# Kernel tuning notes

Measured on AMD Instinct MI355X. Metric: run time of the kernel, lower is better.

The kernel has to match this reference:

```python
import jax, jax.numpy as jnp
import numpy as np

TOP_K = 32
LN_EPS = 1e-5
NORM_EPS = 1e-12


def _l2_normalize(x):
    # matches F.normalize(x, dim=-1): x / max(||x||_2, eps)
    n = jnp.sqrt(jnp.sum(x * x, axis=-1, keepdims=True))
    return x / jnp.maximum(n, NORM_EPS)


def setup_inputs() -> dict:
    key = jax.random.key(0)
    k1, k2, k3 = jax.random.split(key, 3)
    N, M, D = 8192, 32768, 1024
    return {
        "query": jax.random.normal(k1, (N, D), dtype=jnp.float32),
        "memory_keys": jax.random.normal(k2, (M, D), dtype=jnp.float32) * 0.1,
        "memory_values": jax.random.normal(k3, (M, D), dtype=jnp.float32) * 0.1,
        "temperature": jnp.asarray(1.0 / np.sqrt(D), dtype=jnp.float32),
        "ln_gamma": jnp.ones((D,), dtype=jnp.float32),
        "ln_beta": jnp.zeros((D,), dtype=jnp.float32),
    }


def reference(query, memory_keys, memory_values, temperature, ln_gamma, ln_beta):
    qn = _l2_normalize(query)                       # [N, D]
    kn = _l2_normalize(memory_keys)                 # [M, D]
    sim = jnp.einsum("nd,md->nm", qn, kn) * jnp.abs(temperature)  # [N, M]
    top_scores, top_idx = jax.lax.top_k(sim, TOP_K)               # [N, K]
    attn = jax.nn.softmax(top_scores, axis=-1)                    # [N, K]
    selected = memory_values[top_idx]                             # [N, K, D]
    retrieved = jnp.einsum("nk,nkd->nd", attn, selected)          # [N, D]
    x = retrieved + query
    mu = jnp.mean(x, axis=-1, keepdims=True)
    var = jnp.mean((x - mu) ** 2, axis=-1, keepdims=True)
    out = (x - mu) * jax.lax.rsqrt(var + LN_EPS) * ln_gamma + ln_beta
    return out, attn
```

## Files before the change

### kernel.cpp

```cpp
#include <hip/hip_runtime.h>
#include <hip/hip_bf16.h>

#define D 1024
#define NQ 8192
#define NM 32768
#define TOPK 32
#define NBXT 256

typedef __attribute__((ext_vector_type(8))) __bf16 bf16x8;
typedef __attribute__((ext_vector_type(4))) float f32x4;
typedef __attribute__((ext_vector_type(2))) long longx2;

__device__ __forceinline__ void load_lds16(const void* g, void* l) {
  __builtin_amdgcn_global_load_lds(
      (const __attribute__((address_space(1))) void*)g,
      (__attribute__((address_space(3))) void*)l, 16, 0, 0);
}

__device__ __forceinline__ ushort f2bf(float f) {
  unsigned u = __float_as_uint(f);
  unsigned r = (u + 0x7FFFu + ((u >> 16) & 1u)) >> 16;
  return (ushort)r;
}
__device__ __forceinline__ unsigned key16(unsigned u) {
  return u ^ ((u & 0x8000u) ? 0xFFFFu : 0x8000u);
}
__device__ __forceinline__ float bf2f(ushort u) {
  return __uint_as_float(((unsigned)u) << 16);
}

#define FP8_SCALE 32.0f
#define INV_ACC (1.0f / 1024.0f)

__global__ __launch_bounds__(256) void norm_cast8_k(const float* __restrict__ in,
                                                    unsigned* __restrict__ out8) {
  const int row = blockIdx.x;
  const int tid = threadIdx.x;
  const float4 v = ((const float4*)(in + (size_t)row * D))[tid];
  float ss = v.x * v.x + v.y * v.y + v.z * v.z + v.w * v.w;
#pragma unroll
  for (int off = 32; off; off >>= 1) ss += __shfl_xor(ss, off, 64);
  __shared__ float wsum[4];
  const int wid = tid >> 6, lane = tid & 63;
  if (lane == 0) wsum[wid] = ss;
  __syncthreads();
  const float tot = wsum[0] + wsum[1] + wsum[2] + wsum[3];
  const float inv = FP8_SCALE / fmaxf(sqrtf(tot), 1e-12f);
  int r = __builtin_amdgcn_cvt_pk_fp8_f32(v.x * inv, v.y * inv, 0, false);
  r = __builtin_amdgcn_cvt_pk_fp8_f32(v.z * inv, v.w * inv, r, true);
  const int w5 = tid & 31, blk = tid >> 5;
  const int g = w5 >> 1;
  const int h = g >> 2, l4g = g & 3;
  const int G = (h >> 1) * 8 + l4g * 2 + (h & 1);
  out8[(size_t)row * 256 + blk * 32 + G * 2 + (w5 & 1)] = (unsigned)r;
}

__global__ __launch_bounds__(256) void cast_v_k(const float* __restrict__ in,
                                                ushort* __restrict__ out) {
  const int row = blockIdx.x;
  const int tid = threadIdx.x;
  const float4 v = ((const float4*)(in + (size_t)row * D))[tid];
  ushort4 o;
  o.x = f2bf(v.x);
  o.y = f2bf(v.y);
  o.z = f2bf(v.z);
  o.w = f2bf(v.w);
  ((ushort4*)(out + (size_t)row * D))[tid] = o;
}

__global__ __launch_bounds__(256, 4) void gemm128(const uchar* __restrict__ A8,
                                                  const uchar* __restrict__ B8,
                                                  ushort* __restrict__ C,
                                                  ushort* __restrict__ TM,
                                                  int nby, int srows) {
  __shared__ alignas(16) ushort lds[16384];
  __shared__ float wmax[2][128];
  uchar* const As = (uchar*)lds;
  uchar* const Bs = (uchar*)lds + 16384;
  const int tid = threadIdx.x;
  const int lane = tid & 63, wid = tid >> 6;
  const int l15 = lane & 15, l4 = lane >> 4;

  const int nwg = (int)gridDim.x;
  const int q = nwg >> 3, r = nwg & 7;
  const int xcd = (int)blockIdx.x & 7, pos = (int)blockIdx.x >> 3;
  const int wg = (xcd < r ? xcd * (q + 1) : r * (q + 1) + (xcd - r) * q) + pos;
  const int bx = wg / nby, by = wg % nby;

  const int wr = wid >> 1, wc = wid & 1;

  f32x4 acc[4][4];
#pragma unroll
  for (int m = 0; m < 4; m++)
#pragma unroll
    for (int n = 0; n < 4; n++) acc[m][n] = f32x4{0.f, 0.f, 0.f, 0.f};

  const int srow = tid >> 3;
  const int cc = ((tid & 7) ^ ((tid >> 3) & 7)) << 4;
  const uchar* gA = A8 + ((size_t)by * 128 + srow) * 1024 + cc;
  const uchar* gB = B8 + ((size_t)bx * 128 + srow) * 1024 + cc;
  uchar* const ldsA = As + wid * 1024;
  uchar* const ldsB = Bs + wid * 1024;

  const int ob0 = (((0 + l4) ^ (l15 & 7)) << 4);
  const int ob1 = (((4 + l4) ^ (l15 & 7)) << 4);
  const uchar* const abase = As + (wr * 64 + l15) * 128;
  const uchar* const bbase = Bs + (wc * 64 + l15) * 128;

#pragma unroll 1
  for (int kt = 0; kt < 8; ++kt) {
    const int ko = kt * 128;
#pragma unroll
    for (int l = 0; l < 4; ++l) {
      load_lds16(gA + (size_t)l * 32 * 1024 + ko, ldsA + l * 4096);
      load_lds16(gB + (size_t)l * 32 * 1024 + ko, ldsB + l * 4096);
    }
    __syncthreads();
#pragma unroll
    for (int hp = 0; hp < 2; ++hp) {
      const int ob = hp ? ob1 : ob0;
      longx2 af[4], bfv[4];
#pragma unroll
      for (int m = 0; m < 4; ++m) af[m] = *(const longx2*)(abase + m * 2048 + ob);
#pragma unroll
      for (int n = 0; n < 4; ++n) bfv[n] = *(const longx2*)(bbase + n * 2048 + ob);
#pragma unroll
      for (int m = 0; m < 4; ++m)
#pragma unroll
        for (int n = 0; n < 4; ++n) {
          acc[m][n] = __builtin_amdgcn_mfma_f32_16x16x32_fp8_fp8(af[m].x, bfv[n].x, acc[m][n], 0, 0, 0);
          acc[m][n] = __builtin_amdgcn_mfma_f32_16x16x32_fp8_fp8(af[m].y, bfv[n].y, acc[m][n], 0, 0, 0);
        }
    }
    __syncthreads();
  }

#pragma unroll
  for (int m = 0; m < 4; ++m)
#pragma unroll
    for (int j = 0; j < 4; ++j) {
      float fm = fmaxf(fmaxf(acc[m][0][j], acc[m][1][j]), fmaxf(acc[m][2][j], acc[m][3][j]));
#pragma unroll
      for (int off = 1; off < 16; off <<= 1) fm = fmaxf(fm, __shfl_xor(fm, off, 64));
      if (l15 == 0) wmax[wc][wr * 64 + l4 * 4 + m * 16 + j] = fm;
    }
  __syncthreads();
  if (tid < 128) {
    const float fm = fmaxf(wmax[0][tid], wmax[1][tid]) * INV_ACC;
    TM[(size_t)bx * srows + by * 128 + tid] = (ushort)key16((unsigned)f2bf(fm));
  }

#pragma unroll
  for (int m = 0; m < 4; ++m)
#pragma unroll
    for (int n = 0; n < 4; ++n) {
      const int col = wc * 64 + n * 16 + l15;
      const int c8 = col >> 3, c7 = col & 7;
#pragma unroll
      for (int j = 0; j < 4; ++j) {
        const int row = wr * 64 + m * 16 + l4 * 4 + j;
        lds[row * 128 + ((c8 ^ (row & 7)) << 3) + c7] = f2bf(acc[m][n][j] * INV_ACC);
      }
    }
  __syncthreads();
  const int orow = tid >> 4, seg = tid & 15;
#pragma unroll
  for (int p = 0; p < 8; ++p) {
    const int row = p * 16 + orow;
    const bf16x8 v = *(const bf16x8*)&lds[row * 128 + ((seg ^ (row & 7)) << 3)];
    *(bf16x8*)&C[((size_t)by * 128 + row) * NM + bx * 128 + seg * 8] = v;
  }
}

#define CAP2 1024
__global__ __launch_bounds__(512) void topk_k(const ushort* __restrict__ scores,
                                              const ushort* __restrict__ tmax,
                                              int srows, int row_base,
                                              const float* __restrict__ temp,
                                              float* __restrict__ attn,
                                              int* __restrict__ idx_out) {
  const int lrow = blockIdx.x;
  const int grow = row_base + lrow;
  const int tid = threadIdx.x;
  const int lane = tid & 63, wid = tid >> 6;
  __shared__ unsigned tlb_s, M_s;
  __shared__ int nqt_s, cnt_s;
  __shared__ ushort qt[NBXT];
  __shared__ unsigned ckey[CAP2];
  __shared__ unsigned cand64[64];
  __shared__ unsigned okey[TOPK];
  __shared__ int oidx[TOPK];

  if (tid == 0) cnt_s = 0;

  if (tid < 64) {
    const unsigned k0 = tmax[(size_t)lane * srows + lrow];
    const unsigned k1 = tmax[(size_t)(lane + 64) * srows + lrow];
    const unsigned k2 = tmax[(size_t)(lane + 128) * srows + lrow];
    const unsigned k3 = tmax[(size_t)(lane + 192) * srows + lrow];
    unsigned mx = max(max(k0, k1), max(k2, k3));
#pragma unroll
    for (int off = 32; off; off >>= 1) mx = max(mx, __shfl_xor(mx, off, 64));
    unsigned lo = 0, hi = mx;
    while (lo < hi) {
      const unsigned mid = (lo + hi + 1) >> 1;
      int c = (int)(k0 >= mid) + (int)(k1 >= mid) + (int)(k2 >= mid) + (int)(k3 >= mid);
#pragma unroll
      for (int off = 32; off; off >>= 1) c += __shfl_xor(c, off, 64);
      if (c >= TOPK) lo = mid; else hi = mid - 1;
    }
    int base = 0;
    {
      const bool p = k0 >= lo;
      const unsigned long long bm = __ballot(p);
      if (p) qt[base + __popcll(bm & ((1ull << lane) - 1ull))] = (ushort)lane;
      base += __popcll(bm);
    }
    {
      const bool p = k1 >= lo;
      const unsigned long long bm = __ballot(p);
      if (p) qt[base + __popcll(bm & ((1ull << lane) - 1ull))] = (ushort)(lane + 64);
      base += __popcll(bm);
    }
    {
      const bool p = k2 >= lo;
      const unsigned long long bm = __ballot(p);
      if (p) qt[base + __popcll(bm & ((1ull << lane) - 1ull))] = (ushort)(lane + 128);
      base += __popcll(bm);
    }
    {
      const bool p = k3 >= lo;
      const unsigned long long bm = __ballot(p);
      if (p) qt[base + __popcll(bm & ((1ull << lane) - 1ull))] = (ushort)(lane + 192);
      base += __popcll(bm);
    }
    if (lane == 0) { nqt_s = base; tlb_s = lo; M_s = mx; }
  }
  __syncthreads();
  const unsigned M = M_s;
  const int nqt = nqt_s;
  unsigned t0 = tlb_s;
  unsigned tlo = t0, thi = M;

  const unsigned* rowu = (const unsigned*)(scores + (size_t)lrow * NM);
  int cnt = 0;
  for (int att = 0; att < 18; ++att) {
    for (int i = wid; i < nqt; i += 8) {
      const int tb = qt[i];
      const unsigned u = rowu[tb * 64 + lane];
      const unsigned m = (u >> 15) & 0x00010001u;
      const unsigned kk = u ^ (m * 0x7FFFu + 0x80008000u);
      const unsigned klo = kk & 0xFFFFu, khi = kk >> 16;
      const int bidx = tb * 128 + lane * 2;
      if (klo >= t0) { const int qq = atomicAdd(&cnt_s, 1); if (qq < CAP2) ckey[qq] = (klo << 16) | (unsigned)(32767 - bidx); }
      if (khi >= t0) { const int qq = atomicAdd(&cnt_s, 1); if (qq < CAP2) ckey[qq] = (khi << 16) | (unsigned)(32767 - (bidx + 1)); }
    }
    __syncthreads();
    cnt = cnt_s;
    __syncthreads();
    if ((cnt >= TOPK && cnt <= CAP2) || att == 17) break;
    if (cnt > CAP2) { tlo = t0; t0 = t0 + ((thi - t0 + 1) >> 1); }
    else { thi = t0; t0 = tlo + ((t0 - tlo) >> 1); }
    if (tid == 0) cnt_s = 0;
    __syncthreads();
  }
  const int n = min(cnt, CAP2);

  if (tid < 64) {
    unsigned lo = t0, hi = M;
    while (lo < hi) {
      const unsigned mid = (lo + hi + 1) >> 1;
      int c = 0;
      for (int i = lane; i < n; i += 64) c += (int)((ckey[i] >> 16) >= mid);
#pragma unroll
      for (int off = 32; off; off >>= 1) c += __shfl_xor(c, off, 64);
      if (c >= TOPK) lo = mid; else hi = mid - 1;
    }
    const unsigned t32 = lo;
    int c32 = 0;
    for (int i = lane; i < n; i += 64) c32 += (int)((ckey[i] >> 16) >= t32);
#pragma unroll
    for (int off = 32; off; off >>= 1) c32 += __shfl_xor(c32, off, 64);

    if (c32 <= 64) {
      cand64[lane] = 0;
      int base = 0;
      for (int r0 = 0; r0 < n; r0 += 64) {
        const int i = r0 + lane;
        const unsigned k = (i < n) ? ckey[i] : 0u;
        const bool p = (k >> 16) >= t32;
        const unsigned long long bm = __ballot(p);
        if (p) {
          const int ps = base + __popcll(bm & ((1ull << lane) - 1ull));
          if (ps < 64) cand64[ps] = k;
        }
        base += __popcll(bm);
      }
      unsigned v = cand64[lane];
#pragma unroll
      for (int k2 = 2; k2 <= 64; k2 <<= 1) {
#pragma unroll
        for (int j = k2 >> 1; j > 0; j >>= 1) {
          const unsigned o = __shfl_xor(v, j, 64);
          const bool lower = (lane & j) == 0;
          const bool descB = (lane & k2) == 0;
          const unsigned mxv = v > o ? v : o;
          const unsigned mnv = v > o ? o : v;
          v = (lower == descB) ? mxv : mnv;
        }
      }
      if (lane < TOPK) {
        okey[lane] = v >> 16;
        oidx[lane] = 32767 - (int)(v & 0x7FFFu);
      }
    } else {
      for (int k = 0; k < TOPK; ++k) {
        unsigned bk = 0;
        for (int j = lane; j < n; j += 64) bk = max(bk, ckey[j]);
#pragma unroll
        for (int off = 32; off; off >>= 1) bk = max(bk, __shfl_xor(bk, off, 64));
        if (lane == 0) {
          okey[k] = bk >> 16;
          oidx[k] = 32767 - (int)(bk & 0x7FFFu);
        }
        for (int j = lane; j < n; j += 64)
          if (ckey[j] == bk) ckey[j] = 0;
      }
    }
  }
  __syncthreads();

  if (tid < TOPK) {
    const float T = fabsf(temp[0]);
    const unsigned k0 = okey[tid];
    const unsigned u0 = (k0 & 0x8000u) ? (k0 ^ 0x8000u) : (k0 ^ 0xFFFFu);
    const unsigned km = okey[0];
    const unsigned um = (km & 0x8000u) ? (km ^ 0x8000u) : (km ^ 0xFFFFu);
    const float s = __uint_as_float(u0 << 16) * T;
    const float mx = __uint_as_float(um << 16) * T;
    const float e = __expf(s - mx);
    float sum = e;
#pragma unroll
    for (int off = 16; off; off >>= 1) sum += __shfl_xor(sum, off, 32);
    attn[(size_t)grow * TOPK + tid] = e / sum;
    idx_out[(size_t)grow * TOPK + tid] = oidx[tid];
  }
}

__global__ __launch_bounds__(256) void gather_ln_bf(const ushort* __restrict__ V16,
                                                    const float* __restrict__ Q,
                                                    const float* __restrict__ gamma,
                                                    const float* __restrict__ beta,
                                                    const float* __restrict__ attn,
                                                    const int* __restrict__ idx,
                                                    float* __restrict__ out) {
  const int tid = threadIdx.x;
  const int rh = tid >> 7;
  const int t7 = tid & 127;
  const int row = blockIdx.x * 2 + rh;
  __shared__ float a_s[2][TOPK];
  __shared__ int i_s[2][TOPK];
  __shared__ float redS[2][2], redQ[2][2];
  if (t7 < TOPK) {
    a_s[rh][t7] = attn[(size_t)row * TOPK + t7];
    i_s[rh][t7] = idx[(size_t)row * TOPK + t7];
  }
  __syncthreads();

  const int e0 = t7 * 8;
  float acc[8];
#pragma unroll
  for (int u = 0; u < 8; ++u) acc[u] = 0.f;
#pragma unroll
  for (int kb = 0; kb < TOPK; kb += 8) {
    bf16x8 v[8];
#pragma unroll
    for (int u = 0; u < 8; ++u)
      v[u] = *(const bf16x8*)&V16[(size_t)i_s[rh][kb + u] * D + e0];
#pragma unroll
    for (int u = 0; u < 8; ++u) {
      const float a = a_s[rh][kb + u];
      const ushort* vu = (const ushort*)&v[u];
#pragma unroll
      for (int c = 0; c < 8; ++c) acc[c] = fmaf(a, bf2f(vu[c]), acc[c]);
    }
  }

  const float4 q0 = *(const float4*)&Q[(size_t)row * D + e0];
  const float4 q1 = *(const float4*)&Q[(size_t)row * D + e0 + 4];
  float x[8] = {acc[0] + q0.x, acc[1] + q0.y, acc[2] + q0.z, acc[3] + q0.w,
                acc[4] + q1.x, acc[5] + q1.y, acc[6] + q1.z, acc[7] + q1.w};
  float s = 0.f, ss = 0.f;
#pragma unroll
  for (int c = 0; c < 8; ++c) { s += x[c]; ss += x[c] * x[c]; }
#pragma unroll
  for (int off = 32; off; off >>= 1) {
    s += __shfl_xor(s, off, 64);
    ss += __shfl_xor(ss, off, 64);
  }
  const int w2 = (t7 >> 6);
  if ((tid & 63) == 0) { redS[rh][w2] = s; redQ[rh][w2] = ss; }
  __syncthreads();
  const float S = redS[rh][0] + redS[rh][1];
  const float SS = redQ[rh][0] + redQ[rh][1];
  const float mu = S * (1.0f / D);
  const float var = SS * (1.0f / D) - mu * mu;
  const float rstd = rsqrtf(var + 1e-5f);
  const float4 g0 = *(const float4*)&gamma[e0];
  const float4 g1 = *(const float4*)&gamma[e0 + 4];
  const float4 b0 = *(const float4*)&beta[e0];
  const float4 b1 = *(const float4*)&beta[e0 + 4];
  const float g[8] = {g0.x, g0.y, g0.z, g0.w, g1.x, g1.y, g1.z, g1.w};
  const float b[8] = {b0.x, b0.y, b0.z, b0.w, b1.x, b1.y, b1.z, b1.w};
  float4 o0, o1;
  o0.x = (x[0] - mu) * rstd * g[0] + b[0];
  o0.y = (x[1] - mu) * rstd * g[1] + b[1];
  o0.z = (x[2] - mu) * rstd * g[2] + b[2];
  o0.w = (x[3] - mu) * rstd * g[3] + b[3];
  o1.x = (x[4] - mu) * rstd * g[4] + b[4];
  o1.y = (x[5] - mu) * rstd * g[5] + b[5];
  o1.z = (x[6] - mu) * rstd * g[6] + b[6];
  o1.w = (x[7] - mu) * rstd * g[7] + b[7];
  *(float4*)&out[(size_t)row * D + e0] = o0;
  *(float4*)&out[(size_t)row * D + e0 + 4] = o1;
}

__global__ __launch_bounds__(256) void gather_ln_k(const float* __restrict__ V,
                                                   const float* __restrict__ Q,
                                                   const float* __restrict__ gamma,
                                                   const float* __restrict__ beta,
                                                   const float* __restrict__ attn,
                                                   const int* __restrict__ idx,
                                                   float* __restrict__ out) {
  const int row = blockIdx.x, tid = threadIdx.x;
  __shared__ float a_s[TOPK];
  __shared__ int i_s[TOPK];
  __shared__ float redS[4], redQ[4];
  if (tid < TOPK) {
    a_s[tid] = attn[(size_t)row * TOPK + tid];
    i_s[tid] = idx[(size_t)row * TOPK + tid];
  }
  __syncthreads();
  float4 acc = {0.f, 0.f, 0.f, 0.f};
#pragma unroll
  for (int kb = 0; kb < TOPK; kb += 8) {
    float4 v[8];
#pragma unroll
    for (int u = 0; u < 8; ++u)
      v[u] = ((const float4*)(V + (size_t)i_s[kb + u] * D))[tid];
#pragma unroll
    for (int u = 0; u < 8; ++u) {
      const float a = a_s[kb + u];
      acc.x = fmaf(a, v[u].x, acc.x);
      acc.y = fmaf(a, v[u].y, acc.y);
      acc.z = fmaf(a, v[u].z, acc.z);
      acc.w = fmaf(a, v[u].w, acc.w);
    }
  }
  const float4 q = ((const float4*)(Q + (size_t)row * D))[tid];
  float4 x = {acc.x + q.x, acc.y + q.y, acc.z + q.z, acc.w + q.w};
  float s = x.x + x.y + x.z + x.w;
  float ss = x.x * x.x + x.y * x.y + x.z * x.z + x.w * x.w;
#pragma unroll
  for (int off = 32; off; off >>= 1) {
    s += __shfl_xor(s, off, 64);
    ss += __shfl_xor(ss, off, 64);
  }
  const int wid = tid >> 6, lane = tid & 63;
  if (lane == 0) { redS[wid] = s; redQ[wid] = ss; }
  __syncthreads();
  const float S = redS[0] + redS[1] + redS[2] + redS[3];
  const float SS = redQ[0] + redQ[1] + redQ[2] + redQ[3];
  const float mu = S * (1.0f / D);
  const float var = SS * (1.0f / D) - mu * mu;
  const float rstd = rsqrtf(var + 1e-5f);
  const float4 g = ((const float4*)gamma)[tid];
  const float4 b = ((const float4*)beta)[tid];
  float4 o;
  o.x = (x.x - mu) * rstd * g.x + b.x;
  o.y = (x.y - mu) * rstd * g.y + b.y;
  o.z = (x.z - mu) * rstd * g.z + b.z;
  o.w = (x.w - mu) * rstd * g.w + b.w;
  ((float4*)(out + (size_t)row * D))[tid] = o;
}

extern "C" void kernel_launch(void* const* d_in, const int* in_sizes, int n_in,
                              void* d_out, int out_size, void* d_ws, size_t ws_size,
                              hipStream_t stream) {
  const float* Q = (const float*)d_in[0];
  const float* K = (const float*)d_in[1];
  const float* V = (const float*)d_in[2];
  const float* T = (const float*)d_in[3];
  const float* G = (const float*)d_in[4];
  const float* Bt = (const float*)d_in[5];
  float* out = (float*)d_out;
  float* attn = out + (size_t)NQ * D;

  char* ws = (char*)d_ws;
  const size_t off_q8 = 0;
  const size_t off_k8 = off_q8 + (size_t)NQ * D;
  const size_t off_idx = off_k8 + (size_t)NM * D;
  const size_t off_tm = off_idx + (size_t)NQ * TOPK * sizeof(int);
  const size_t off_v16 = off_tm + (size_t)NBXT * 2048 * 2;
  const size_t v16_bytes = (size_t)NM * D * 2;

  const bool use_v16 = ws_size >= off_v16 + v16_bytes + (size_t)256 * NM * 2;
  const size_t off_sc = use_v16 ? off_v16 + v16_bytes : off_v16;

  unsigned* q8 = (unsigned*)(ws + off_q8);
  unsigned* k8 = (unsigned*)(ws + off_k8);
  int* idx = (int*)(ws + off_idx);
  ushort* tm = (ushort*)(ws + off_tm);
  ushort* v16 = (ushort*)(ws + off_v16);
  ushort* scores = (ushort*)(ws + off_sc);

  const size_t avail = ws_size > off_sc ? ws_size - off_sc : 0;
  int slice = 2048;
  while (slice > 256 && (size_t)slice * NM * 2ull > avail) slice >>= 1;

  norm_cast8_k<<<NQ, 256, 0, stream>>>(Q, q8);
  norm_cast8_k<<<NM, 256, 0, stream>>>(K, k8);
  if (use_v16) cast_v_k<<<NM, 256, 0, stream>>>(V, v16);

  const int nbx = NM / 128;
  for (int s0 = 0; s0 < NQ; s0 += slice) {
    const int nby = slice / 128;
    gemm128<<<nbx * nby, 256, 0, stream>>>((const uchar*)q8 + (size_t)s0 * D,
                                           (const uchar*)k8, scores, tm, nby, slice);
    topk_k<<<slice, 512, 0, stream>>>(scores, tm, slice, s0, T, attn, idx);
  }
  if (use_v16)
    gather_ln_bf<<<NQ / 2, 256, 0, stream>>>(v16, Q, G, Bt, attn, idx, out);
  else
    gather_ln_k<<<NQ, 256, 0, stream>>>(V, Q, G, Bt, attn, idx, out);
}
```

Before: 666.3 us.

## Double-buffer GEMM LDS staging and store gathered values as FP8

The fp8 GEMM now double-buffers its LDS tiles, issuing the global-to-LDS loads for the next K tile before computing on the current one. This removes one barrier per iteration and overlaps load latency with MFMA work, at the cost of twice the LDS and a launch-bounds occupancy hint lowered from 4 to 2. Separately, memory values are cast to scaled FP8 instead of bf16, which halves cast-write and gather-read traffic but lowers the precision of the retrieved vectors.

```diff
diff --git a/kernel.cpp b/kernel.cpp
--- a/kernel.cpp
+++ b/kernel.cpp
@@ -25,12 +25,11 @@
 __device__ __forceinline__ unsigned key16(unsigned u) {
   return u ^ ((u & 0x8000u) ? 0xFFFFu : 0x8000u);
 }
-__device__ __forceinline__ float bf2f(ushort u) {
-  return __uint_as_float(((unsigned)u) << 16);
-}
 
 #define FP8_SCALE 32.0f
 #define INV_ACC (1.0f / 1024.0f)
+#define V8_SCALE 16.0f
+#define INV_V8 (1.0f / 16.0f)
 
 __global__ __launch_bounds__(256) void norm_cast8_k(const float* __restrict__ in,
                                                     unsigned* __restrict__ out8) {
@@ -55,28 +54,25 @@
   out8[(size_t)row * 256 + blk * 32 + G * 2 + (w5 & 1)] = (unsigned)r;
 }
 
-__global__ __launch_bounds__(256) void cast_v_k(const float* __restrict__ in,
-                                                ushort* __restrict__ out) {
+__global__ __launch_bounds__(256) void cast_v8_k(const float* __restrict__ in,
+                                                 unsigned* __restrict__ out8) {
   const int row = blockIdx.x;
   const int tid = threadIdx.x;
   const float4 v = ((const float4*)(in + (size_t)row * D))[tid];
-  ushort4 o;
-  o.x = f2bf(v.x);
-  o.y = f2bf(v.y);
-  o.z = f2bf(v.z);
-  o.w = f2bf(v.w);
-  ((ushort4*)(out + (size_t)row * D))[tid] = o;
-}
-
-__global__ __launch_bounds__(256, 4) void gemm128(const uchar* __restrict__ A8,
+  int r = __builtin_amdgcn_cvt_pk_fp8_f32(v.x * V8_SCALE, v.y * V8_SCALE, 0, false);
+  r = __builtin_amdgcn_cvt_pk_fp8_f32(v.z * V8_SCALE, v.w * V8_SCALE, r, true);
+  out8[(size_t)row * 256 + tid] = (unsigned)r;
+}
+
+__global__ __launch_bounds__(256, 2) void gemm128(const uchar* __restrict__ A8,
                                                   const uchar* __restrict__ B8,
                                                   ushort* __restrict__ C,
                                                   ushort* __restrict__ TM,
                                                   int nby, int srows) {
-  __shared__ alignas(16) ushort lds[16384];
+  __shared__ alignas(16) ushort lds[32768];
   __shared__ float wmax[2][128];
-  uchar* const As = (uchar*)lds;
-  uchar* const Bs = (uchar*)lds + 16384;
+  uchar* const AS = (uchar*)lds;
+  uchar* const BS = (uchar*)lds + 32768;
   const int tid = threadIdx.x;
   const int lane = tid & 63, wid = tid >> 6;
   const int l15 = lane & 15, l4 = lane >> 4;
@@ -99,23 +95,30 @@
   const int cc = ((tid & 7) ^ ((tid >> 3) & 7)) << 4;
   const uchar* gA = A8 + ((size_t)by * 128 + srow) * 1024 + cc;
   const uchar* gB = B8 + ((size_t)bx * 128 + srow) * 1024 + cc;
-  uchar* const ldsA = As + wid * 1024;
-  uchar* const ldsB = Bs + wid * 1024;
+
+#define STAGE8(tt, b)                                                     \
+  do {                                                                    \
+    const int ko_ = (tt) * 128;                                           \
+    uchar* const dA_ = AS + (b) * 16384 + wid * 1024;                     \
+    uchar* const dB_ = BS + (b) * 16384 + wid * 1024;                     \
+    _Pragma("unroll") for (int l_ = 0; l_ < 4; ++l_) {                    \
+      load_lds16(gA + (size_t)l_ * 32 * 1024 + ko_, dA_ + l_ * 4096);     \
+      load_lds16(gB + (size_t)l_ * 32 * 1024 + ko_, dB_ + l_ * 4096);     \
+    }                                                                     \
+  } while (0)
 
   const int ob0 = (((0 + l4) ^ (l15 & 7)) << 4);
   const int ob1 = (((4 + l4) ^ (l15 & 7)) << 4);
-  const uchar* const abase = As + (wr * 64 + l15) * 128;
-  const uchar* const bbase = Bs + (wc * 64 + l15) * 128;
+
+  STAGE8(0, 0);
+  __syncthreads();
 
 #pragma unroll 1
   for (int kt = 0; kt < 8; ++kt) {
-    const int ko = kt * 128;
-#pragma unroll
-    for (int l = 0; l < 4; ++l) {
-      load_lds16(gA + (size_t)l * 32 * 1024 + ko, ldsA + l * 4096);
-      load_lds16(gB + (size_t)l * 32 * 1024 + ko, ldsB + l * 4096);
-    }
-    __syncthreads();
+    const int b = kt & 1;
+    if (kt < 7) STAGE8(kt + 1, b ^ 1);
+    const uchar* const abase = AS + b * 16384 + (wr * 64 + l15) * 128;
+    const uchar* const bbase = BS + b * 16384 + (wc * 64 + l15) * 128;
 #pragma unroll
     for (int hp = 0; hp < 2; ++hp) {
       const int ob = hp ? ob1 : ob0;
@@ -134,6 +137,7 @@
     }
     __syncthreads();
   }
+#undef STAGE8
 
 #pragma unroll
   for (int m = 0; m < 4; ++m)
@@ -347,7 +351,7 @@
   }
 }
 
-__global__ __launch_bounds__(256) void gather_ln_bf(const ushort* __restrict__ V16,
+__global__ __launch_bounds__(256) void gather_ln_f8(const uchar* __restrict__ V8,
                                                     const float* __restrict__ Q,
                                                     const float* __restrict__ gamma,
                                                     const float* __restrict__ beta,
@@ -373,23 +377,30 @@
   for (int u = 0; u < 8; ++u) acc[u] = 0.f;
 #pragma unroll
   for (int kb = 0; kb < TOPK; kb += 8) {
-    bf16x8 v[8];
+    uint2 v[8];
 #pragma unroll
     for (int u = 0; u < 8; ++u)
-      v[u] = *(const bf16x8*)&V16[(size_t)i_s[rh][kb + u] * D + e0];
+      v[u] = *(const uint2*)&V8[(size_t)i_s[rh][kb + u] * D + e0];
 #pragma unroll
     for (int u = 0; u < 8; ++u) {
       const float a = a_s[rh][kb + u];
-      const ushort* vu = (const ushort*)&v[u];
-#pragma unroll
-      for (int c = 0; c < 8; ++c) acc[c] = fmaf(a, bf2f(vu[c]), acc[c]);
+      acc[0] = fmaf(a, __builtin_amdgcn_cvt_f32_fp8((int)v[u].x, 0), acc[0]);
+      acc[1] = fmaf(a, __builtin_amdgcn_cvt_f32_fp8((int)v[u].x, 1), acc[1]);
+      acc[2] = fmaf(a, __builtin_amdgcn_cvt_f32_fp8((int)v[u].x, 2), acc[2]);
+      acc[3] = fmaf(a, __builtin_amdgcn_cvt_f32_fp8((int)v[u].x, 3), acc[3]);
+      acc[4] = fmaf(a, __builtin_amdgcn_cvt_f32_fp8((int)v[u].y, 0), acc[4]);
+      acc[5] = fmaf(a, __builtin_amdgcn_cvt_f32_fp8((int)v[u].y, 1), acc[5]);
+      acc[6] = fmaf(a, __builtin_amdgcn_cvt_f32_fp8((int)v[u].y, 2), acc[6]);
+      acc[7] = fmaf(a, __builtin_amdgcn_cvt_f32_fp8((int)v[u].y, 3), acc[7]);
     }
   }
 
   const float4 q0 = *(const float4*)&Q[(size_t)row * D + e0];
   const float4 q1 = *(const float4*)&Q[(size_t)row * D + e0 + 4];
-  float x[8] = {acc[0] + q0.x, acc[1] + q0.y, acc[2] + q0.z, acc[3] + q0.w,
-                acc[4] + q1.x, acc[5] + q1.y, acc[6] + q1.z, acc[7] + q1.w};
+  float x[8] = {acc[0] * INV_V8 + q0.x, acc[1] * INV_V8 + q0.y,
+                acc[2] * INV_V8 + q0.z, acc[3] * INV_V8 + q0.w,
+                acc[4] * INV_V8 + q1.x, acc[5] * INV_V8 + q1.y,
+                acc[6] * INV_V8 + q1.z, acc[7] * INV_V8 + q1.w};
   float s = 0.f, ss = 0.f;
 #pragma unroll
   for (int c = 0; c < 8; ++c) { s += x[c]; ss += x[c] * x[c]; }
@@ -501,17 +512,17 @@
   const size_t off_k8 = off_q8 + (size_t)NQ * D;
   const size_t off_idx = off_k8 + (size_t)NM * D;
   const size_t off_tm = off_idx + (size_t)NQ * TOPK * sizeof(int);
-  const size_t off_v16 = off_tm + (size_t)NBXT * 2048 * 2;
-  const size_t v16_bytes = (size_t)NM * D * 2;
-
-  const bool use_v16 = ws_size >= off_v16 + v16_bytes + (size_t)256 * NM * 2;
-  const size_t off_sc = use_v16 ? off_v16 + v16_bytes : off_v16;
+  const size_t off_v8 = off_tm + (size_t)NBXT * 2048 * 2;
+  const size_t v8_bytes = (size_t)NM * D;
+
+  const bool use_v8 = ws_size >= off_v8 + v8_bytes + (size_t)256 * NM * 2;
+  const size_t off_sc = use_v8 ? off_v8 + v8_bytes : off_v8;
 
   unsigned* q8 = (unsigned*)(ws + off_q8);
   unsigned* k8 = (unsigned*)(ws + off_k8);
   int* idx = (int*)(ws + off_idx);
   ushort* tm = (ushort*)(ws + off_tm);
-  ushort* v16 = (ushort*)(ws + off_v16);
+  unsigned* v8 = (unsigned*)(ws + off_v8);
   ushort* scores = (ushort*)(ws + off_sc);
 
   const size_t avail = ws_size > off_sc ? ws_size - off_sc : 0;
@@ -520,7 +531,7 @@
 
   norm_cast8_k<<<NQ, 256, 0, stream>>>(Q, q8);
   norm_cast8_k<<<NM, 256, 0, stream>>>(K, k8);
-  if (use_v16) cast_v_k<<<NM, 256, 0, stream>>>(V, v16);
+  if (use_v8) cast_v8_k<<<NM, 256, 0, stream>>>(V, v8);
 
   const int nbx = NM / 128;
   for (int s0 = 0; s0 < NQ; s0 += slice) {
@@ -529,8 +540,8 @@
                                            (const uchar*)k8, scores, tm, nby, slice);
     topk_k<<<slice, 512, 0, stream>>>(scores, tm, slice, s0, T, attn, idx);
   }
-  if (use_v16)
-    gather_ln_bf<<<NQ / 2, 256, 0, stream>>>(v16, Q, G, Bt, attn, idx, out);
+  if (use_v8)
+    gather_ln_f8<<<NQ / 2, 256, 0, stream>>>((const uchar*)v8, Q, G, Bt, attn, idx, out);
   else
     gather_ln_k<<<NQ, 256, 0, stream>>>(V, Q, G, Bt, attn, idx, out);
 }
```

Result: slower. 749.5 us (+12.5%).
